# Performance work log

Measured on AMD Instinct MI355X. Metric: run time of the kernel, lower is better.

Reference implementation:

```python
import jax, jax.numpy as jnp
import numpy as np
from math import sqrt

LOCAL_WINDOW = 32
STRIDE = 64


def _sparse_mask(L):
    # L_Q == L_K path of DozerAttention:
    #  - local window: diagonals at offsets 0..local_window//2 (both signs)
    #  - strided: diagonals at offsets 0, stride+1, 2*(stride+1), ... (both signs)
    i = jnp.arange(L)[:, None]
    j = jnp.arange(L)[None, :]
    d = jnp.abs(i - j)
    local = d <= (LOCAL_WINDOW // 2)
    strided = (d % (STRIDE + 1)) == 0
    return (local | strided).astype(jnp.float32)  # [L, L]


def setup_inputs() -> dict:
    key = jax.random.key(0)
    B, L, H, D = 2, 2048, 8, 64
    kq, kk, kv = jax.random.split(key, 3)
    queries = jax.random.normal(kq, (B, L, H, D), dtype=jnp.float32)
    keys = jax.random.normal(kk, (B, L, H, D), dtype=jnp.float32)
    values = jax.random.normal(kv, (B, L, H, D), dtype=jnp.float32)
    # TriangularCausalMask: True above the diagonal -> masked with -inf
    causal = jnp.triu(jnp.ones((L, L), dtype=bool), k=1)
    attn_mask = jnp.broadcast_to(causal[None, None], (B, 1, L, L))
    return {"queries": queries, "keys": keys, "values": values, "attn_mask": attn_mask}


def reference(queries, keys, values, attn_mask):
    B, L, H, D = queries.shape
    scale = 1.0 / sqrt(D)
    sm = _sparse_mask(L)  # [L, L]
    # Original fills a zero-initialized dense score tensor only at selected key
    # columns per query row; equivalent to dense QK^T elementwise-masked by sm
    # (non-selected entries stay exactly 0, NOT -inf -- faithful quirk).
    scores = jnp.einsum('blhe,bshe->bhls', queries, keys) * sm  # [B,H,L,L]
    scores = jnp.where(attn_mask, -jnp.inf, scores)
    A = jax.nn.softmax(scale * scores, axis=-1)  # dropout p=0.0 in this config
    V = jnp.einsum('bhls,bshd->blhd', A, values)  # [B,L,H,D]
    return V
```

## Files before the change

kernel.cpp:

```cpp
#include <hip/hip_runtime.h>
#include <hip/hip_bf16.h>

#define B_ 2
#define L_ 2048
#define H_ 8
#define D_ 64
#define SP_ 65
#define NC_ 128
#define RS_ 512

typedef __attribute__((ext_vector_type(8))) short bf16x8;
typedef __attribute__((ext_vector_type(16))) float f32x16;

static __device__ inline short f2bf(float x) {
    return __builtin_bit_cast(short, __float2bfloat16(x));
}

static __device__ inline bf16x8 ld8_bf16(const float* __restrict__ p) {
    float4 a = *(const float4*)p;
    float4 b = *(const float4*)(p + 4);
    bf16x8 r;
    r[0]=f2bf(a.x); r[1]=f2bf(a.y); r[2]=f2bf(a.z); r[3]=f2bf(a.w);
    r[4]=f2bf(b.x); r[5]=f2bf(b.y); r[6]=f2bf(b.z); r[7]=f2bf(b.w);
    return r;
}

static __device__ inline bf16x8 ones_frag() {
    bf16x8 r;
    short o = f2bf(1.f);
    #pragma unroll
    for (int t = 0; t < 8; ++t) r[t] = o;
    return r;
}

__global__ __launch_bounds__(256) void partials_k(const float* __restrict__ q,
                                                  const float* __restrict__ kk,
                                                  const float* __restrict__ v,
                                                  float* __restrict__ csum1,
                                                  float* __restrict__ pA,
                                                  float* __restrict__ zA,
                                                  float* __restrict__ pB,
                                                  float* __restrict__ zB) {
    __shared__ float LDS[4608];
    int wib  = threadIdx.x >> 6;
    int lane = threadIdx.x & 63;
    int half = lane >> 5, ln = lane & 31;
    int blk  = blockIdx.x;

    if (blk < 512) {
        int tb = wib >> 1;
        int hf = wib & 1;
        int team = blk * 2 + tb;
        int bh = team >> 6;
        int T  = (team & 63) << 5;
        int h = bh & 7, b = bh >> 3;
        const size_t base = (size_t)b * L_ * RS_ + (size_t)h * D_;
        float* Pw = LDS + tb * 2176;
        int d0 = 32 * hf;

        bf16x8 bv[4];
        #pragma unroll
        for (int kb = 0; kb < 4; ++kb) {
            #pragma unroll
            for (int jj = 0; jj < 8; ++jj) {
                int jr = T - 16 + kb * 16 + half * 8 + jj;
                jr = jr < 0 ? 0 : (jr > L_ - 1 ? L_ - 1 : jr);
                bv[kb][jj] = f2bf(v[base + (size_t)jr * RS_ + d0 + ln]);
            }
        }

        const float* qrow = q + base + (size_t)(T + ln) * RS_;
        bf16x8 aq[4];
        #pragma unroll
        for (int kb = 0; kb < 4; ++kb) aq[kb] = ld8_bf16(qrow + kb * 16 + half * 8);

        int j = T - 16 + d0 + ln;
        j = j < 0 ? 0 : (j > L_ - 1 ? L_ - 1 : j);
        const float* krow = kk + base + (size_t)j * RS_;
        f32x16 acc = {};
        #pragma unroll
        for (int kb = 0; kb < 4; ++kb) {
            bf16x8 kf = ld8_bf16(krow + kb * 16 + half * 8);
            acc = __builtin_amdgcn_mfma_f32_32x32x16_bf16(aq[kb], kf, acc, 0, 0, 0);
        }

        #pragma unroll
        for (int r = 0; r < 16; ++r) {
            int m = (r & 3) + 8 * (r >> 2) + 4 * half;
            float w;
            if (hf == 0) {
                bool act = (ln >= m) && (ln <= m + 16) && (T - 16 + ln >= 0);
                w = act ? (__expf(0.125f * acc[r]) - 1.f) : 0.f;
                if ((m < 16) && (ln >= 16) && (ln <= m + 16)) w += 1.f;
            } else {
                bool act = (ln <= m - 16);
                w = act ? (__expf(0.125f * acc[r]) - 1.f) : 0.f;
                if ((m >= 16) && (ln <= m - 16)) w += 1.f;
            }
            Pw[m * 68 + d0 + ln] = w;
        }
        __syncthreads();

        f32x16 p = {}; f32x16 po = {};
        bf16x8 ones = ones_frag();
        #pragma unroll
        for (int kb = 0; kb < 4; ++kb) {
            int k0 = kb * 16 + half * 8;
            const float* pr = &Pw[ln * 68 + k0];
            float4 x = *(const float4*)pr;
            float4 y = *(const float4*)(pr + 4);
            bf16x8 ap;
            ap[0]=f2bf(x.x); ap[1]=f2bf(x.y); ap[2]=f2bf(x.z); ap[3]=f2bf(x.w);
            ap[4]=f2bf(y.x); ap[5]=f2bf(y.y); ap[6]=f2bf(y.z); ap[7]=f2bf(y.w);
            p = __builtin_amdgcn_mfma_f32_32x32x16_bf16(ap, bv[kb], p, 0, 0, 0);
            if (hf == 1)
                po = __builtin_amdgcn_mfma_f32_32x32x16_bf16(ap, ones, po, 0, 0, 0);
        }

        float* pAr = pA + (size_t)bh * L_ * D_;
        float* zAr = zA + (size_t)bh * L_;
        #pragma unroll
        for (int r = 0; r < 16; ++r) {
            int m = (r & 3) + 8 * (r >> 2) + 4 * half;
            int i = T + m;
            pAr[(size_t)i * D_ + d0 + ln] = p[r];
            if (hf == 1 && ln == 0)
                zAr[i] = po[r] - (float)((m & 15) + 1);
        }
    } else if (blk < 772) {
        int us = (blk - 512) * 4 + wib;
        int bh = us / SP_;
        int r  = us % SP_;
        int h = bh & 7, b = bh >> 3;
        const size_t base = (size_t)b * L_ * RS_ + (size_t)h * D_;
        float* Pw = LDS + wib * 1152;

        bf16x8 bv0[2], bv1[2];
        #pragma unroll
        for (int kb = 0; kb < 2; ++kb) {
            int k0 = kb * 16 + half * 8;
            #pragma unroll
            for (int jj = 0; jj < 8; ++jj) {
                int lv = r + SP_ * (k0 + jj);
                lv = lv > L_ - 1 ? L_ - 1 : lv;
                const float* vr = v + base + (size_t)lv * RS_;
                bv0[kb][jj] = f2bf(vr[ln]);
                bv1[kb][jj] = f2bf(vr[32 + ln]);
            }
        }

        int lq = r + SP_ * ln;
        int lqc = lq > L_ - 1 ? L_ - 1 : lq;
        const float* qrow = q  + base + (size_t)lqc * RS_;
        const float* krow = kk + base + (size_t)lqc * RS_;
        f32x16 acc = {};
        #pragma unroll
        for (int kb = 0; kb < 4; ++kb) {
            bf16x8 a  = ld8_bf16(qrow + kb * 16 + half * 8);
            bf16x8 bb = ld8_bf16(krow + kb * 16 + half * 8);
            acc = __builtin_amdgcn_mfma_f32_32x32x16_bf16(a, bb, acc, 0, 0, 0);
        }
        #pragma unroll
        for (int rg = 0; rg < 16; ++rg) {
            int m = (rg & 3) + 8 * (rg >> 2) + 4 * half;
            bool act = (ln < m) && (r + SP_ * m < L_);
            Pw[m * 36 + ln] = act ? (__expf(0.125f * acc[rg]) - 1.f) : 0.f;
        }
        __syncthreads();

        f32x16 p0 = {}; f32x16 p1 = {}; f32x16 po = {};
        bf16x8 ones = ones_frag();
        #pragma unroll
        for (int kb = 0; kb < 2; ++kb) {
            int k0 = kb * 16 + half * 8;
            const float* pr = &Pw[ln * 36 + k0];
            float4 x = *(const float4*)pr;
            float4 y = *(const float4*)(pr + 4);
            bf16x8 ap;
            ap[0]=f2bf(x.x); ap[1]=f2bf(x.y); ap[2]=f2bf(x.z); ap[3]=f2bf(x.w);
            ap[4]=f2bf(y.x); ap[5]=f2bf(y.y); ap[6]=f2bf(y.z); ap[7]=f2bf(y.w);
            p0 = __builtin_amdgcn_mfma_f32_32x32x16_bf16(ap, bv0[kb], p0, 0, 0, 0);
            p1 = __builtin_amdgcn_mfma_f32_32x32x16_bf16(ap, bv1[kb], p1, 0, 0, 0);
            po = __builtin_amdgcn_mfma_f32_32x32x16_bf16(ap, ones,    po, 0, 0, 0);
        }
        float* pBr = pB + (size_t)bh * L_ * D_;
        float* zBr = zB + (size_t)bh * L_;
        #pragma unroll
        for (int rg = 0; rg < 16; ++rg) {
            int m = (rg & 3) + 8 * (rg >> 2) + 4 * half;
            int l = r + SP_ * m;
            if (l < L_) {
                pBr[(size_t)l * D_ + ln]      = p0[rg];
                pBr[(size_t)l * D_ + 32 + ln] = p1[rg];
                if (ln == 0) zBr[l] = po[rg];
            }
        }
    } else {
        int uc = (blk - 772) * 4 + wib;
        int c = uc & (NC_ - 1);
        int bh = uc >> 7;
        int h = bh & 7, b = bh >> 3;
        const float* vb = v + (size_t)(b * L_ + c * 16) * RS_ + h * D_ + lane;
        float s = 0.f;
        #pragma unroll
        for (int l = 0; l < 16; ++l) s += vb[l * RS_];
        csum1[(size_t)uc * D_ + lane] = s;
    }
}

__global__ __launch_bounds__(256) void combine_k(const float* __restrict__ csum1,
                                                 const float* __restrict__ pA,
                                                 const float* __restrict__ zA,
                                                 const float* __restrict__ pB,
                                                 const float* __restrict__ zB,
                                                 float* __restrict__ out) {
    int wib  = threadIdx.x >> 6;
    int lane = threadIdx.x & 63;
    int u = blockIdx.x * 4 + wib;
    int bh = u >> 8;
    int g  = u & 255;
    int i0 = g << 3;
    int c1 = i0 >> 4;
    int h = bh & 7, b = bh >> 3;

    const float* zAr = zA + (size_t)bh * L_;
    const float* zBr = zB + (size_t)bh * L_;
    float zsum[8];
    #pragma unroll
    for (int r = 0; r < 8; ++r) {
        int i = i0 + r;
        zsum[r] = zAr[i] + zBr[i] + (float)(i + 1);
    }

    const float* cs1 = csum1 + (size_t)bh * NC_ * D_ + lane;
    float s0 = 0.f, s1 = 0.f, s2 = 0.f, s3 = 0.f;
    int cc = 0;
    for (; cc + 4 <= c1; cc += 4) {
        s0 += cs1[(cc + 0) * D_]; s1 += cs1[(cc + 1) * D_];
        s2 += cs1[(cc + 2) * D_]; s3 += cs1[(cc + 3) * D_];
    }
    for (; cc < c1; ++cc) s0 += cs1[cc * D_];
    float pr = (s0 + s1) + (s2 + s3);

    const float* pAr = pA + (size_t)bh * L_ * D_;
    const float* pBr = pB + (size_t)bh * L_ * D_;
    const size_t obase = (size_t)b * L_ * RS_ + (size_t)h * D_;

    #pragma unroll
    for (int r = 0; r < 8; ++r) {
        int i = i0 + r;
        float num = pAr[(size_t)i * D_ + lane] + pBr[(size_t)i * D_ + lane] + pr;
        out[obase + (size_t)i * RS_ + lane] = num / zsum[r];
    }
}

extern "C" void kernel_launch(void* const* d_in, const int* in_sizes, int n_in,
                              void* d_out, int out_size, void* d_ws, size_t ws_size,
                              hipStream_t stream) {
    const float* q = (const float*)d_in[0];
    const float* k = (const float*)d_in[1];
    const float* v = (const float*)d_in[2];
    float* out = (float*)d_out;

    float* csum1 = (float*)d_ws;
    float* pA    = csum1 + (size_t)B_ * H_ * NC_ * D_;
    float* zA    = pA    + (size_t)B_ * H_ * L_ * D_;
    float* pB    = zA    + (size_t)B_ * H_ * L_;
    float* zB    = pB    + (size_t)B_ * H_ * L_ * D_;

    partials_k<<<1284, 256, 0, stream>>>(q, k, v, csum1, pA, zA, pB, zB);
    combine_k<<<1024, 256, 0, stream>>>(csum1, pA, zA, pB, zB, out);
}
```

Measured before the change: 110.2 us.

## Fuse partials and combine into one cooperative kernel with grid sync

Merges the two kernels into a single cooperative launch of 512 blocks. Each block's first two waves compute the local-window partials for a 32-row tile and keep them in LDS rather than writing pA/zA to global memory. The other two waves handle the strided partials and the column sums. After a grid-wide sync, every block combines its own LDS tile with the global strided partials and prefix sums and writes the output. This removes one kernel launch and the global round trip for pA/zA. In exchange it adds a grid barrier, uneven work between wave roles, and a lower grid size with higher LDS use per block.

```diff
diff --git a/kernel.cpp b/kernel.cpp
--- a/kernel.cpp
+++ b/kernel.cpp
@@ -1,5 +1,6 @@
 #include <hip/hip_runtime.h>
 #include <hip/hip_bf16.h>
+#include <hip/hip_cooperative_groups.h>
 
 #define B_ 2
 #define L_ 2048
@@ -33,39 +34,36 @@
     return r;
 }
 
-__global__ __launch_bounds__(256) void partials_k(const float* __restrict__ q,
+__global__ __launch_bounds__(256, 2) void fused_k(const float* __restrict__ q,
                                                   const float* __restrict__ kk,
                                                   const float* __restrict__ v,
                                                   float* __restrict__ csum1,
-                                                  float* __restrict__ pA,
-                                                  float* __restrict__ zA,
                                                   float* __restrict__ pB,
-                                                  float* __restrict__ zB) {
-    __shared__ float LDS[4608];
+                                                  float* __restrict__ zB,
+                                                  float* __restrict__ out) {
+    __shared__ float LDS[8704];
     int wib  = threadIdx.x >> 6;
     int lane = threadIdx.x & 63;
     int half = lane >> 5, ln = lane & 31;
-    int blk  = blockIdx.x;
-
-    if (blk < 512) {
-        int tb = wib >> 1;
-        int hf = wib & 1;
-        int team = blk * 2 + tb;
+    float* Pw = LDS + wib * 2176;
+
+    if (wib < 2) {
+        int team = blockIdx.x * 2 + wib;
         int bh = team >> 6;
         int T  = (team & 63) << 5;
         int h = bh & 7, b = bh >> 3;
         const size_t base = (size_t)b * L_ * RS_ + (size_t)h * D_;
-        float* Pw = LDS + tb * 2176;
-        int d0 = 32 * hf;
-
-        bf16x8 bv[4];
+
+        bf16x8 bv0[4], bv1[4];
         #pragma unroll
         for (int kb = 0; kb < 4; ++kb) {
             #pragma unroll
             for (int jj = 0; jj < 8; ++jj) {
                 int jr = T - 16 + kb * 16 + half * 8 + jj;
                 jr = jr < 0 ? 0 : (jr > L_ - 1 ? L_ - 1 : jr);
-                bv[kb][jj] = f2bf(v[base + (size_t)jr * RS_ + d0 + ln]);
+                const float* vr = v + base + (size_t)jr * RS_;
+                bv0[kb][jj] = f2bf(vr[ln]);
+                bv1[kb][jj] = f2bf(vr[32 + ln]);
             }
         }
 
@@ -74,106 +72,39 @@
         #pragma unroll
         for (int kb = 0; kb < 4; ++kb) aq[kb] = ld8_bf16(qrow + kb * 16 + half * 8);
 
-        int j = T - 16 + d0 + ln;
-        j = j < 0 ? 0 : (j > L_ - 1 ? L_ - 1 : j);
-        const float* krow = kk + base + (size_t)j * RS_;
-        f32x16 acc = {};
-        #pragma unroll
-        for (int kb = 0; kb < 4; ++kb) {
-            bf16x8 kf = ld8_bf16(krow + kb * 16 + half * 8);
-            acc = __builtin_amdgcn_mfma_f32_32x32x16_bf16(aq[kb], kf, acc, 0, 0, 0);
-        }
-
-        #pragma unroll
-        for (int r = 0; r < 16; ++r) {
-            int m = (r & 3) + 8 * (r >> 2) + 4 * half;
-            float w;
-            if (hf == 0) {
-                bool act = (ln >= m) && (ln <= m + 16) && (T - 16 + ln >= 0);
-                w = act ? (__expf(0.125f * acc[r]) - 1.f) : 0.f;
-                if ((m < 16) && (ln >= 16) && (ln <= m + 16)) w += 1.f;
-            } else {
-                bool act = (ln <= m - 16);
-                w = act ? (__expf(0.125f * acc[r]) - 1.f) : 0.f;
-                if ((m >= 16) && (ln <= m - 16)) w += 1.f;
-            }
-            Pw[m * 68 + d0 + ln] = w;
-        }
-        __syncthreads();
-
-        f32x16 p = {}; f32x16 po = {};
-        bf16x8 ones = ones_frag();
-        #pragma unroll
-        for (int kb = 0; kb < 4; ++kb) {
-            int k0 = kb * 16 + half * 8;
-            const float* pr = &Pw[ln * 68 + k0];
-            float4 x = *(const float4*)pr;
-            float4 y = *(const float4*)(pr + 4);
-            bf16x8 ap;
-            ap[0]=f2bf(x.x); ap[1]=f2bf(x.y); ap[2]=f2bf(x.z); ap[3]=f2bf(x.w);
-            ap[4]=f2bf(y.x); ap[5]=f2bf(y.y); ap[6]=f2bf(y.z); ap[7]=f2bf(y.w);
-            p = __builtin_amdgcn_mfma_f32_32x32x16_bf16(ap, bv[kb], p, 0, 0, 0);
-            if (hf == 1)
-                po = __builtin_amdgcn_mfma_f32_32x32x16_bf16(ap, ones, po, 0, 0, 0);
-        }
-
-        float* pAr = pA + (size_t)bh * L_ * D_;
-        float* zAr = zA + (size_t)bh * L_;
-        #pragma unroll
-        for (int r = 0; r < 16; ++r) {
-            int m = (r & 3) + 8 * (r >> 2) + 4 * half;
-            int i = T + m;
-            pAr[(size_t)i * D_ + d0 + ln] = p[r];
-            if (hf == 1 && ln == 0)
-                zAr[i] = po[r] - (float)((m & 15) + 1);
-        }
-    } else if (blk < 772) {
-        int us = (blk - 512) * 4 + wib;
-        int bh = us / SP_;
-        int r  = us % SP_;
-        int h = bh & 7, b = bh >> 3;
-        const size_t base = (size_t)b * L_ * RS_ + (size_t)h * D_;
-        float* Pw = LDS + wib * 1152;
-
-        bf16x8 bv0[2], bv1[2];
-        #pragma unroll
-        for (int kb = 0; kb < 2; ++kb) {
-            int k0 = kb * 16 + half * 8;
-            #pragma unroll
-            for (int jj = 0; jj < 8; ++jj) {
-                int lv = r + SP_ * (k0 + jj);
-                lv = lv > L_ - 1 ? L_ - 1 : lv;
-                const float* vr = v + base + (size_t)lv * RS_;
-                bv0[kb][jj] = f2bf(vr[ln]);
-                bv1[kb][jj] = f2bf(vr[32 + ln]);
-            }
-        }
-
-        int lq = r + SP_ * ln;
-        int lqc = lq > L_ - 1 ? L_ - 1 : lq;
-        const float* qrow = q  + base + (size_t)lqc * RS_;
-        const float* krow = kk + base + (size_t)lqc * RS_;
-        f32x16 acc = {};
-        #pragma unroll
-        for (int kb = 0; kb < 4; ++kb) {
-            bf16x8 a  = ld8_bf16(qrow + kb * 16 + half * 8);
-            bf16x8 bb = ld8_bf16(krow + kb * 16 + half * 8);
-            acc = __builtin_amdgcn_mfma_f32_32x32x16_bf16(a, bb, acc, 0, 0, 0);
-        }
-        #pragma unroll
-        for (int rg = 0; rg < 16; ++rg) {
-            int m = (rg & 3) + 8 * (rg >> 2) + 4 * half;
-            bool act = (ln < m) && (r + SP_ * m < L_);
-            Pw[m * 36 + ln] = act ? (__expf(0.125f * acc[rg]) - 1.f) : 0.f;
-        }
-        __syncthreads();
+        #pragma unroll
+        for (int ct = 0; ct < 2; ++ct) {
+            int j = T - 16 + 32 * ct + ln;
+            j = j < 0 ? 0 : (j > L_ - 1 ? L_ - 1 : j);
+            const float* krow = kk + base + (size_t)j * RS_;
+            f32x16 acc = {};
+            #pragma unroll
+            for (int kb = 0; kb < 4; ++kb) {
+                bf16x8 kf = ld8_bf16(krow + kb * 16 + half * 8);
+                acc = __builtin_amdgcn_mfma_f32_32x32x16_bf16(aq[kb], kf, acc, 0, 0, 0);
+            }
+            #pragma unroll
+            for (int r = 0; r < 16; ++r) {
+                int m = (r & 3) + 8 * (r >> 2) + 4 * half;
+                float w;
+                if (ct == 0) {
+                    bool act = (ln >= m) && (ln <= m + 16) && (T - 16 + ln >= 0);
+                    w = act ? (__expf(0.125f * acc[r]) - 1.f) : 0.f;
+                    if ((m < 16) && (ln >= 16) && (ln <= m + 16)) w += 1.f;
+                } else {
+                    bool act = (ln <= m - 16);
+                    w = act ? (__expf(0.125f * acc[r]) - 1.f) : 0.f;
+                    if ((m >= 16) && (ln <= m - 16)) w += 1.f;
+                }
+                Pw[m * 68 + 32 * ct + ln] = w;
+            }
+        }
 
         f32x16 p0 = {}; f32x16 p1 = {}; f32x16 po = {};
         bf16x8 ones = ones_frag();
         #pragma unroll
-        for (int kb = 0; kb < 2; ++kb) {
-            int k0 = kb * 16 + half * 8;
-            const float* pr = &Pw[ln * 36 + k0];
+        for (int kb = 0; kb < 4; ++kb) {
+            const float* pr = &Pw[ln * 68 + kb * 16 + half * 8];
             float4 x = *(const float4*)pr;
             float4 y = *(const float4*)(pr + 4);
             bf16x8 ap;
@@ -183,74 +114,135 @@
             p1 = __builtin_amdgcn_mfma_f32_32x32x16_bf16(ap, bv1[kb], p1, 0, 0, 0);
             po = __builtin_amdgcn_mfma_f32_32x32x16_bf16(ap, ones,    po, 0, 0, 0);
         }
-        float* pBr = pB + (size_t)bh * L_ * D_;
-        float* zBr = zB + (size_t)bh * L_;
-        #pragma unroll
-        for (int rg = 0; rg < 16; ++rg) {
-            int m = (rg & 3) + 8 * (rg >> 2) + 4 * half;
-            int l = r + SP_ * m;
-            if (l < L_) {
-                pBr[(size_t)l * D_ + ln]      = p0[rg];
-                pBr[(size_t)l * D_ + 32 + ln] = p1[rg];
-                if (ln == 0) zBr[l] = po[rg];
-            }
+
+        #pragma unroll
+        for (int r = 0; r < 16; ++r) {
+            int m = (r & 3) + 8 * (r >> 2) + 4 * half;
+            Pw[m * 68 + ln]      = p0[r];
+            Pw[m * 68 + 32 + ln] = p1[r];
+            if (ln == 0) Pw[m * 68 + 64] = po[r];
         }
     } else {
-        int uc = (blk - 772) * 4 + wib;
-        int c = uc & (NC_ - 1);
-        int bh = uc >> 7;
+        int sw = blockIdx.x * 2 + (wib - 2);
+        #pragma unroll 1
+        for (int rep = 0; rep < 2; ++rep) {
+            if (rep == 1 && sw >= 16) break;
+            int us = (rep == 0) ? sw : 1024 + sw;
+            int bh = us / SP_;
+            int r  = us % SP_;
+            int h = bh & 7, b = bh >> 3;
+            const size_t base = (size_t)b * L_ * RS_ + (size_t)h * D_;
+
+            bf16x8 bv0[2], bv1[2];
+            #pragma unroll
+            for (int kb = 0; kb < 2; ++kb) {
+                int k0 = kb * 16 + half * 8;
+                #pragma unroll
+                for (int jj = 0; jj < 8; ++jj) {
+                    int lv = r + SP_ * (k0 + jj);
+                    lv = lv > L_ - 1 ? L_ - 1 : lv;
+                    const float* vr = v + base + (size_t)lv * RS_;
+                    bv0[kb][jj] = f2bf(vr[ln]);
+                    bv1[kb][jj] = f2bf(vr[32 + ln]);
+                }
+            }
+
+            int lq = r + SP_ * ln;
+            int lqc = lq > L_ - 1 ? L_ - 1 : lq;
+            const float* qrow = q  + base + (size_t)lqc * RS_;
+            const float* krow = kk + base + (size_t)lqc * RS_;
+            f32x16 acc = {};
+            #pragma unroll
+            for (int kb = 0; kb < 4; ++kb) {
+                bf16x8 a  = ld8_bf16(qrow + kb * 16 + half * 8);
+                bf16x8 bb = ld8_bf16(krow + kb * 16 + half * 8);
+                acc = __builtin_amdgcn_mfma_f32_32x32x16_bf16(a, bb, acc, 0, 0, 0);
+            }
+            #pragma unroll
+            for (int rg = 0; rg < 16; ++rg) {
+                int m = (rg & 3) + 8 * (rg >> 2) + 4 * half;
+                bool act = (ln < m) && (r + SP_ * m < L_);
+                Pw[m * 36 + ln] = act ? (__expf(0.125f * acc[rg]) - 1.f) : 0.f;
+            }
+
+            f32x16 p0 = {}; f32x16 p1 = {}; f32x16 po = {};
+            bf16x8 ones = ones_frag();
+            #pragma unroll
+            for (int kb = 0; kb < 2; ++kb) {
+                const float* pr = &Pw[ln * 36 + kb * 16 + half * 8];
+                float4 x = *(const float4*)pr;
+                float4 y = *(const float4*)(pr + 4);
+                bf16x8 ap;
+                ap[0]=f2bf(x.x); ap[1]=f2bf(x.y); ap[2]=f2bf(x.z); ap[3]=f2bf(x.w);
+                ap[4]=f2bf(y.x); ap[5]=f2bf(y.y); ap[6]=f2bf(y.z); ap[7]=f2bf(y.w);
+                p0 = __builtin_amdgcn_mfma_f32_32x32x16_bf16(ap, bv0[kb], p0, 0, 0, 0);
+                p1 = __builtin_amdgcn_mfma_f32_32x32x16_bf16(ap, bv1[kb], p1, 0, 0, 0);
+                po = __builtin_amdgcn_mfma_f32_32x32x16_bf16(ap, ones,    po, 0, 0, 0);
+            }
+            float* pBr = pB + (size_t)bh * L_ * D_;
+            float* zBr = zB + (size_t)bh * L_;
+            #pragma unroll
+            for (int rg = 0; rg < 16; ++rg) {
+                int m = (rg & 3) + 8 * (rg >> 2) + 4 * half;
+                int l = r + SP_ * m;
+                if (l < L_) {
+                    pBr[(size_t)l * D_ + ln]      = p0[rg];
+                    pBr[(size_t)l * D_ + 32 + ln] = p1[rg];
+                    if (ln == 0) zBr[l] = po[rg];
+                }
+            }
+        }
+
+        #pragma unroll 1
+        for (int t = 0; t < 2; ++t) {
+            int uc = sw * 2 + t;
+            int c  = uc & (NC_ - 1);
+            int bh = uc >> 7;
+            int h = bh & 7, b = bh >> 3;
+            const float* vb = v + (size_t)(b * L_ + c * 16) * RS_ + h * D_ + lane;
+            float s = 0.f;
+            #pragma unroll
+            for (int l = 0; l < 16; ++l) s += vb[l * RS_];
+            csum1[(size_t)uc * D_ + lane] = s;
+        }
+    }
+
+    cooperative_groups::this_grid().sync();
+
+    {
+        int team = blockIdx.x * 2 + (wib & 1);
+        int m0   = (wib >> 1) << 4;
+        int bh = team >> 6;
+        int T  = (team & 63) << 5;
         int h = bh & 7, b = bh >> 3;
-        const float* vb = v + (size_t)(b * L_ + c * 16) * RS_ + h * D_ + lane;
-        float s = 0.f;
-        #pragma unroll
-        for (int l = 0; l < 16; ++l) s += vb[l * RS_];
-        csum1[(size_t)uc * D_ + lane] = s;
-    }
-}
-
-__global__ __launch_bounds__(256) void combine_k(const float* __restrict__ csum1,
-                                                 const float* __restrict__ pA,
-                                                 const float* __restrict__ zA,
-                                                 const float* __restrict__ pB,
-                                                 const float* __restrict__ zB,
-                                                 float* __restrict__ out) {
-    int wib  = threadIdx.x >> 6;
-    int lane = threadIdx.x & 63;
-    int u = blockIdx.x * 4 + wib;
-    int bh = u >> 8;
-    int g  = u & 255;
-    int i0 = g << 3;
-    int c1 = i0 >> 4;
-    int h = bh & 7, b = bh >> 3;
-
-    const float* zAr = zA + (size_t)bh * L_;
-    const float* zBr = zB + (size_t)bh * L_;
-    float zsum[8];
-    #pragma unroll
-    for (int r = 0; r < 8; ++r) {
-        int i = i0 + r;
-        zsum[r] = zAr[i] + zBr[i] + (float)(i + 1);
-    }
-
-    const float* cs1 = csum1 + (size_t)bh * NC_ * D_ + lane;
-    float s0 = 0.f, s1 = 0.f, s2 = 0.f, s3 = 0.f;
-    int cc = 0;
-    for (; cc + 4 <= c1; cc += 4) {
-        s0 += cs1[(cc + 0) * D_]; s1 += cs1[(cc + 1) * D_];
-        s2 += cs1[(cc + 2) * D_]; s3 += cs1[(cc + 3) * D_];
-    }
-    for (; cc < c1; ++cc) s0 += cs1[cc * D_];
-    float pr = (s0 + s1) + (s2 + s3);
-
-    const float* pAr = pA + (size_t)bh * L_ * D_;
-    const float* pBr = pB + (size_t)bh * L_ * D_;
-    const size_t obase = (size_t)b * L_ * RS_ + (size_t)h * D_;
-
-    #pragma unroll
-    for (int r = 0; r < 8; ++r) {
-        int i = i0 + r;
-        float num = pAr[(size_t)i * D_ + lane] + pBr[(size_t)i * D_ + lane] + pr;
-        out[obase + (size_t)i * RS_ + lane] = num / zsum[r];
+        const float* PL = LDS + (wib & 1) * 2176;
+        const float* zBr = zB + (size_t)bh * L_;
+
+        float zrow[16];
+        #pragma unroll
+        for (int rr = 0; rr < 16; ++rr) zrow[rr] = zBr[T + m0 + rr];
+
+        int cEnd = (T >> 4) + (m0 ? 1 : 0);
+        const float* cs = csum1 + (size_t)bh * NC_ * D_ + lane;
+        float s0 = 0.f, s1 = 0.f, s2 = 0.f, s3 = 0.f;
+        int c = 0;
+        for (; c + 4 <= cEnd; c += 4) {
+            s0 += cs[(c + 0) * D_]; s1 += cs[(c + 1) * D_];
+            s2 += cs[(c + 2) * D_]; s3 += cs[(c + 3) * D_];
+        }
+        for (; c < cEnd; ++c) s0 += cs[c * D_];
+        float pr = (s0 + s1) + (s2 + s3);
+
+        const float* pBr = pB + (size_t)bh * L_ * D_;
+        const size_t obase = (size_t)b * L_ * RS_ + (size_t)h * D_;
+        #pragma unroll
+        for (int rr = 0; rr < 16; ++rr) {
+            int m = m0 + rr;
+            int i = T + m;
+            float zs  = PL[m * 68 + 64] - (float)((m & 15) + 1) + zrow[rr] + (float)(i + 1);
+            float num = PL[m * 68 + lane] + pBr[(size_t)i * D_ + lane] + pr;
+            out[obase + (size_t)i * RS_ + lane] = num / zs;
+        }
     }
 }
 
@@ -263,11 +255,10 @@
     float* out = (float*)d_out;
 
     float* csum1 = (float*)d_ws;
-    float* pA    = csum1 + (size_t)B_ * H_ * NC_ * D_;
-    float* zA    = pA    + (size_t)B_ * H_ * L_ * D_;
-    float* pB    = zA    + (size_t)B_ * H_ * L_;
+    float* pB    = csum1 + (size_t)B_ * H_ * NC_ * D_;
     float* zB    = pB    + (size_t)B_ * H_ * L_ * D_;
 
-    partials_k<<<1284, 256, 0, stream>>>(q, k, v, csum1, pA, zA, pB, zB);
-    combine_k<<<1024, 256, 0, stream>>>(csum1, pA, zA, pB, zB, out);
-}
+    void* args[] = {(void*)&q, (void*)&k, (void*)&v,
+                    (void*)&csum1, (void*)&pB, (void*)&zB, (void*)&out};
+    hipLaunchCooperativeKernel(fused_k, dim3(512), dim3(256), args, 0, stream);
+}
```

Result: slower. 183.4 us (+66.4%).
